# Performance work log

Measured on AMD Instinct MI355X. Metric: run time of the kernel, lower is better.

## Reference

```python
import jax, jax.numpy as jnp
import numpy as np

B, N, E = 32, 256, 300   # batch, num hyperedges, word emb size
H, K = 256, 8            # nhidden, nhead
MARGIN = 0.2


def setup_inputs() -> dict:
    key = jax.random.key(0)
    ks = jax.random.split(key, 10)
    s_in = 1.0 / np.sqrt(E)
    s_h = 1.0 / np.sqrt(H)
    s_fc = 1.0 / np.sqrt(H * K)
    return {
        'he_anchor': jax.random.normal(ks[0], (B, N, E), jnp.float32),
        'he_pos': jax.random.normal(ks[1], (B, N, E), jnp.float32),
        'he_neg': jax.random.normal(ks[2], (B, N, E), jnp.float32),
        'W_a2h': jax.random.uniform(ks[3], (H, E), jnp.float32, -s_in, s_in),
        'b_a2h': jax.random.uniform(ks[4], (H,), jnp.float32, -s_in, s_in),
        'W_c2h': jax.random.uniform(ks[5], (H, E), jnp.float32, -s_in, s_in),
        'b_c2h': jax.random.uniform(ks[6], (H,), jnp.float32, -s_in, s_in),
        'W_att': jax.random.uniform(ks[7], (K, H), jnp.float32, -s_h, s_h),
        'b_att': jax.random.uniform(ks[8], (K,), jnp.float32, -s_h, s_h),
        'W_fc': jax.random.uniform(ks[9], (1, H * K), jnp.float32, -s_fc, s_fc),
        'b_fc': jnp.zeros((1,), jnp.float32),
    }


def _score(x, y, W_a2h, b_a2h, W_c2h, b_c2h, W_att, b_att, W_fc, b_fc):
    # a2h / c2h projections, then permute to [B, H, N]
    Aa = jnp.transpose(x @ W_a2h.T + b_a2h, (0, 2, 1))  # [B,H,N]
    Ac = jnp.transpose(y @ W_c2h.T + b_c2h, (0, 2, 1))  # [B,H,M]
    # h2att applied to the outer product Aa[b,h,n]*Ac[b,h,m]; fuse into one einsum
    logits = jnp.einsum('bhn,bhm,kh->bknm', Aa, Ac, W_att) + b_att[None, :, None, None]
    b_, k_, n_, m_ = logits.shape
    att = jax.nn.softmax(logits.reshape(b_, k_, n_ * m_), axis=-1).reshape(b_, k_, n_, m_)
    # per-head bilinear aggregation: out[b,k,h] = sum_{n,m} Aa[b,h,n]*att[b,k,n,m]*Ac[b,h,m]
    t = jnp.einsum('bhn,bknm->bkhm', Aa, att)
    out = jnp.einsum('bkhm,bhm->bkh', t, Ac)
    # torch concat order is head-major: [B, K*H]
    out = out.reshape(b_, k_ * H)
    return out @ W_fc.T + b_fc  # [B,1]


def reference(he_anchor, he_pos, he_neg, W_a2h, b_a2h, W_c2h, b_c2h, W_att, b_att, W_fc, b_fc):
    score_p = _score(he_anchor, he_pos, W_a2h, b_a2h, W_c2h, b_c2h, W_att, b_att, W_fc, b_fc)
    score_n = _score(he_anchor, he_neg, W_a2h, b_a2h, W_c2h, b_c2h, W_att, b_att, W_fc, b_fc)
    loss = jnp.mean(jax.nn.relu(score_n - score_p + MARGIN))
    return loss
```

## Files before the change

kernel.cpp:

```cpp
#include <hip/hip_runtime.h>

#define BB 32
#define NN 256
#define EE 300
#define HH 256
#define KK 8
#define MARGINF 0.2f
#define EP 320

typedef __attribute__((ext_vector_type(8))) short bf16x8;
typedef __attribute__((ext_vector_type(4))) float f32x4;
typedef __attribute__((ext_vector_type(16))) float f32x16;

__device__ inline ushort f2bf(float f) {
  unsigned u = __float_as_uint(f);
  u += 0x7fffu + ((u >> 16) & 1u);
  return (ushort)(u >> 16);
}
__device__ inline float bf2f(ushort s) { return __uint_as_float(((unsigned)s) << 16); }
__device__ inline unsigned cvtpk(float lo, float hi) {
  unsigned r;
  asm("v_cvt_pk_bf16_f32 %0, %1, %2" : "=v"(r) : "v"(lo), "v"(hi));
  return r;
}
__device__ inline void gload_lds16(const ushort* g, ushort* l) {
  __builtin_amdgcn_global_load_lds(
      (const __attribute__((address_space(1))) void*)g,
      (__attribute__((address_space(3))) void*)l, 16, 0, 0);
}

__global__ __launch_bounds__(256) void wconv_kernel(
    const float* __restrict__ Wa, const float* __restrict__ Wc,
    ushort* __restrict__ Wt, unsigned* __restrict__ counter)
{
  const int i = blockIdx.x * 256 + threadIdx.x;
  if (i == 0) counter[0] = 0u;
  const int w = i / 81920;
  int r = i - w * 81920;
  const int hb = r / 5120; r -= hb * 5120;
  const int ks = r / 512;  r -= ks * 512;
  const int l = r >> 3, j = r & 7;
  const int h = hb * 16 + (l & 15);
  const int e = ks * 32 + (l >> 4) * 8 + j;
  const float* src = w ? Wc : Wa;
  Wt[i] = (e < EE) ? f2bf(src[h * EE + e]) : (ushort)0;
}

__global__ __launch_bounds__(256, 3) void proj_kernel(
    const float* __restrict__ he_a, const float* __restrict__ he_p,
    const float* __restrict__ he_n, const ushort* __restrict__ Wt,
    const float* __restrict__ b_a2h, const float* __restrict__ b_c2h,
    ushort* __restrict__ AT)
{
  const int z = blockIdx.y;
  const int which = z >> 5;
  const int b = z & 31;
  const int nb = blockIdx.x;
  const int n0 = nb * 32;
  const int tid = threadIdx.x;
  const int wv = tid >> 6;
  const int lane = tid & 63;
  const int col = lane & 15;
  const int quad = lane >> 4;

  const float* X = (which == 0 ? he_a : which == 1 ? he_p : he_n) + (size_t)b * NN * EE;
  const ushort* W = Wt + (size_t)(which == 0 ? 0 : 1) * 81920;
  const float* bias = (which == 0 ? b_a2h : b_c2h);

  __shared__ __align__(16) ushort sX[32][328];
  __shared__ __align__(16) ushort tr[32][264];

  {
    const int row = tid >> 3, seg = tid & 7;
    const float* xr = X + (size_t)(n0 + row) * EE;
#pragma unroll
    for (int q = 0; q < 10; q++) {
      const int jj = seg + 8 * q;
      float4 xv = {0.f, 0.f, 0.f, 0.f};
      if (jj < 75) xv = *(const float4*)&xr[4 * jj];
      uint2 p; p.x = cvtpk(xv.x, xv.y); p.y = cvtpk(xv.z, xv.w);
      *(uint2*)&sX[row][4 * jj] = p;
    }
  }
  __syncthreads();

  f32x4 acc[2][4];
#pragma unroll
  for (int nf = 0; nf < 2; nf++)
#pragma unroll
    for (int mb = 0; mb < 4; mb++) acc[nf][mb] = (f32x4){0.f, 0.f, 0.f, 0.f};

#pragma unroll
  for (int ks = 0; ks < 10; ks++) {
    const int off = 32 * ks + 8 * quad;
    const bf16x8 a0 = *(const bf16x8*)&sX[col][off];
    const bf16x8 a1 = *(const bf16x8*)&sX[16 + col][off];
#pragma unroll
    for (int mb = 0; mb < 4; mb++) {
      const bf16x8 w8 = *(const bf16x8*)&W[(4 * wv + mb) * 5120 + ks * 512 + lane * 8];
      acc[0][mb] = __builtin_amdgcn_mfma_f32_16x16x32_bf16(a0, w8, acc[0][mb], 0, 0, 0);
      acc[1][mb] = __builtin_amdgcn_mfma_f32_16x16x32_bf16(a1, w8, acc[1][mb], 0, 0, 0);
    }
  }

#pragma unroll
  for (int nf = 0; nf < 2; nf++)
#pragma unroll
    for (int mb = 0; mb < 4; mb++) {
      const float bi = bias[64 * wv + 16 * mb + col];
#pragma unroll
      for (int r = 0; r < 4; r++)
        tr[16 * nf + 4 * quad + r][64 * wv + 16 * mb + col] = f2bf(acc[nf][mb][r] + bi);
    }
  __syncthreads();
  {
    ushort* dst = AT + (size_t)(which * BB + b) * (NN * HH) + (size_t)nb * 8192;
#pragma unroll
    for (int it = 0; it < 4; it++) {
      const int c = it * 256 + tid;
      const int row = c & 31, hs = (c >> 5) & 1, hb = c >> 6;
      *(uint4*)&dst[c * 8] = *(const uint4*)&tr[row][hb * 16 + hs * 8];
    }
  }
}

__global__ __launch_bounds__(512, 1) void attn_kernel(
    const ushort* __restrict__ AT, const float* __restrict__ Watt,
    const float* __restrict__ Wfc, const float* __restrict__ bfc,
    float* __restrict__ scoresK, unsigned* __restrict__ counter,
    float* __restrict__ out)
{
  const int d = blockIdx.x;
  const int x = d & 7;
  const int j = d >> 3;
  const int grp = x * 8 + (j & 7);
  const int kp = j >> 3;
  const int which = grp >> 5;
  const int b = grp & 31;
  const int tid = threadIdx.x;
  const int wid = tid >> 6;
  const int kh = wid >> 2;
  const int ws = wid & 3;
  const int lane = tid & 63;
  const int k = 2 * kp + kh;

  const ushort* Ta = AT + (size_t)b * (NN * HH);
  const ushort* Tc = AT + (size_t)((1 + which) * BB + b) * (NN * HH);

  __shared__ __align__(16) ushort sB[65536];
  __shared__ __align__(16) ushort wkb[2][256];
  __shared__ __align__(16) ushort wfb[2][256];
  __shared__ float red[16];
  __shared__ unsigned isLast;

#pragma unroll
  for (int it = 0; it < 16; it++) {
    const int off = (wid * 16 + it) * 512;
    gload_lds16(Tc + off + lane * 8, &sB[off]);
  }
  {
    const int h = tid & 255, hd = tid >> 8;
    const int kt = 2 * kp + hd;
    wkb[hd][h] = f2bf(Watt[(size_t)kt * HH + h]);
    wfb[hd][h] = f2bf(Wfc[(size_t)kt * HH + h]);
  }
  __syncthreads();

  const ushort* wkp = wkb[kh];
  const ushort* wfp = wfb[kh];

  float num = 0.f, den = 0.f;

#pragma unroll 1
  for (int si = 0; si < 2; si++) {
    const int s = si ^ kh;
    bf16x8 saf[16], gaf[16];
    {
      const ushort* abase = Ta + (4 * s + ws) * 8192 + lane * 8;
#pragma unroll
      for (int ks = 0; ks < 16; ks++) {
        const bf16x8 a = *(const bf16x8*)&abase[ks * 512];
        const int off = 16 * ks + 8 * (lane >> 5);
        const bf16x8 w8 = *(const bf16x8*)&wkp[off];
        const bf16x8 f8 = *(const bf16x8*)&wfp[off];
        union { bf16x8 v; unsigned u[4]; } sv, gv;
#pragma unroll
        for (int jj = 0; jj < 4; jj++) {
          const float a0 = bf2f((ushort)a[2 * jj]), a1 = bf2f((ushort)a[2 * jj + 1]);
          sv.u[jj] = cvtpk(a0 * bf2f((ushort)w8[2 * jj]), a1 * bf2f((ushort)w8[2 * jj + 1]));
          gv.u[jj] = cvtpk(a0 * bf2f((ushort)f8[2 * jj]), a1 * bf2f((ushort)f8[2 * jj + 1]));
        }
        saf[ks] = sv.v; gaf[ks] = gv.v;
      }
    }

#pragma unroll 1
    for (int mi = 0; mi < 4; mi++) {
      const int mtp = (mi + ws) & 3;
      const int mbase = mtp * 16384;
      f32x16 aS0 = {0,0,0,0,0,0,0,0,0,0,0,0,0,0,0,0};
      f32x16 aG0 = {0,0,0,0,0,0,0,0,0,0,0,0,0,0,0,0};
      f32x16 aS1 = {0,0,0,0,0,0,0,0,0,0,0,0,0,0,0,0};
      f32x16 aG1 = {0,0,0,0,0,0,0,0,0,0,0,0,0,0,0,0};
      __builtin_amdgcn_s_setprio(1);
#pragma unroll
      for (int ks = 0; ks < 16; ks++) {
        const bf16x8 b0 = *(const bf16x8*)&sB[mbase + ks * 512 + lane * 8];
        const bf16x8 b1 = *(const bf16x8*)&sB[mbase + 8192 + ks * 512 + lane * 8];
        aS0 = __builtin_amdgcn_mfma_f32_32x32x16_bf16(saf[ks], b0, aS0, 0, 0, 0);
        aG0 = __builtin_amdgcn_mfma_f32_32x32x16_bf16(gaf[ks], b0, aG0, 0, 0, 0);
        aS1 = __builtin_amdgcn_mfma_f32_32x32x16_bf16(saf[ks], b1, aS1, 0, 0, 0);
        aG1 = __builtin_amdgcn_mfma_f32_32x32x16_bf16(gaf[ks], b1, aG1, 0, 0, 0);
      }
      __builtin_amdgcn_s_setprio(0);
#pragma unroll
      for (int r = 0; r < 16; r++) {
        const float p0 = __expf(aS0[r]);
        den += p0; num = fmaf(p0, aG0[r], num);
        const float p1 = __expf(aS1[r]);
        den += p1; num = fmaf(p1, aG1[r], num);
      }
    }
  }

#pragma unroll
  for (int off = 32; off >= 1; off >>= 1) {
    num += __shfl_xor(num, off);
    den += __shfl_xor(den, off);
  }
  if (lane == 0) { red[wid] = num; red[8 + wid] = den; }
  __syncthreads();
  if (tid == 0) {
    const float n0 = red[0] + red[1] + red[2] + red[3];
    const float d0 = red[8] + red[9] + red[10] + red[11];
    const float n1 = red[4] + red[5] + red[6] + red[7];
    const float d1 = red[12] + red[13] + red[14] + red[15];
    atomicExch(&scoresK[(2 * kp) * 64 + grp], n0 / d0);
    atomicExch(&scoresK[(2 * kp + 1) * 64 + grp], n1 / d1);
    __threadfence();
    isLast = (atomicAdd(counter, 1u) == 255u) ? 1u : 0u;
  }
  __syncthreads();

  if (isLast && tid < 64) {
    float s = bfc[0];
#pragma unroll
    for (int kk = 0; kk < KK; kk++)
      s += atomicAdd(&scoresK[kk * 64 + tid], 0.0f);
    const float other = __shfl(s, tid + 32);
    float v = 0.f;
    if (tid < 32) v = fmaxf(other - s + MARGINF, 0.f);
#pragma unroll
    for (int off = 32; off >= 1; off >>= 1) v += __shfl_xor(v, off);
    if (tid == 0) out[0] = v * (1.0f / 32.0f);
  }
}

extern "C" void kernel_launch(void* const* d_in, const int* in_sizes, int n_in,
                              void* d_out, int out_size, void* d_ws, size_t ws_size,
                              hipStream_t stream) {
  const float* he_a  = (const float*)d_in[0];
  const float* he_p  = (const float*)d_in[1];
  const float* he_n  = (const float*)d_in[2];
  const float* W_a2h = (const float*)d_in[3];
  const float* b_a2h = (const float*)d_in[4];
  const float* W_c2h = (const float*)d_in[5];
  const float* b_c2h = (const float*)d_in[6];
  const float* W_att = (const float*)d_in[7];
  const float* W_fc  = (const float*)d_in[9];
  const float* b_fc  = (const float*)d_in[10];

  ushort* AT = (ushort*)d_ws;
  float* scoresK = (float*)(AT + (size_t)3 * BB * NN * HH);
  ushort* Wt = (ushort*)(scoresK + 512);
  unsigned* counter = (unsigned*)(Wt + (size_t)2 * HH * EP);
  (void)ws_size; (void)in_sizes; (void)n_in; (void)out_size;

  wconv_kernel<<<640, 256, 0, stream>>>(W_a2h, W_c2h, Wt, counter);
  dim3 pg(8, 96);
  proj_kernel<<<pg, 256, 0, stream>>>(he_a, he_p, he_n, Wt, b_a2h, b_c2h, AT);
  attn_kernel<<<256, 512, 0, stream>>>(AT, W_att, W_fc, b_fc, scoresK, counter, (float*)d_out);
}
```

Baseline: 132.5 us.

## Software-pipeline MFMA clusters with exp tails and vectorize weight conversion

The attention kernel's inner loop now computes 32-column MFMA clusters one at a time and overlaps each cluster's MFMAs with the exp/softmax accumulation of the previous cluster, using two ping-pong accumulator pairs. The LDS start offset is rotated per wave across eight clusters. The aim is to hide the VALU exp work behind matrix-core work instead of running them back to back. The weight conversion kernel also handles four elements per thread with float4 loads and launches 4x fewer blocks. The setprio hints were removed, and the ping-pong scheme can raise register pressure.

After: 520.7 us. 3.93x slower.

```diff
diff --git a/kernel.cpp b/kernel.cpp
--- a/kernel.cpp
+++ b/kernel.cpp
@@ -35,15 +35,21 @@
 {
   const int i = blockIdx.x * 256 + threadIdx.x;
   if (i == 0) counter[0] = 0u;
-  const int w = i / 81920;
-  int r = i - w * 81920;
+  const int base = i * 4;
+  const int w = base / 81920;
+  int r = base - w * 81920;
   const int hb = r / 5120; r -= hb * 5120;
   const int ks = r / 512;  r -= ks * 512;
   const int l = r >> 3, j = r & 7;
   const int h = hb * 16 + (l & 15);
-  const int e = ks * 32 + (l >> 4) * 8 + j;
+  const int e0 = ks * 32 + (l >> 4) * 8 + j;
   const float* src = w ? Wc : Wa;
-  Wt[i] = (e < EE) ? f2bf(src[h * EE + e]) : (ushort)0;
+  ushort4 o = {0, 0, 0, 0};
+  if (e0 < EE) {
+    const float4 v = *(const float4*)&src[h * EE + e0];
+    o.x = f2bf(v.x); o.y = f2bf(v.y); o.z = f2bf(v.z); o.w = f2bf(v.w);
+  }
+  *(ushort4*)&Wt[base] = o;
 }
 
 __global__ __launch_bounds__(256, 3) void proj_kernel(
@@ -121,6 +127,29 @@
       const int row = c & 31, hs = (c >> 5) & 1, hb = c >> 6;
       *(uint4*)&dst[c * 8] = *(const uint4*)&tr[row][hb * 16 + hs * 8];
     }
+  }
+}
+
+__device__ __forceinline__ void cluster32(
+    const ushort* sBp, const bf16x8* saf, const bf16x8* gaf,
+    int mbase, int lane, f32x16& aS, f32x16& aG)
+{
+  aS = (f32x16){0,0,0,0,0,0,0,0,0,0,0,0,0,0,0,0};
+  aG = (f32x16){0,0,0,0,0,0,0,0,0,0,0,0,0,0,0,0};
+#pragma unroll
+  for (int ks = 0; ks < 16; ks++) {
+    const bf16x8 bv = *(const bf16x8*)&sBp[mbase + ks * 512 + lane * 8];
+    aS = __builtin_amdgcn_mfma_f32_32x32x16_bf16(saf[ks], bv, aS, 0, 0, 0);
+    aG = __builtin_amdgcn_mfma_f32_32x32x16_bf16(gaf[ks], bv, aG, 0, 0, 0);
+  }
+}
+__device__ __forceinline__ void tail32(
+    const f32x16& aS, const f32x16& aG, float& num, float& den)
+{
+#pragma unroll
+  for (int r = 0; r < 16; r++) {
+    const float p = __expf(aS[r]);
+    den += p; num = fmaf(p, aG[r], num);
   }
 }
 
@@ -142,7 +171,6 @@
   const int kh = wid >> 2;
   const int ws = wid & 3;
   const int lane = tid & 63;
-  const int k = 2 * kp + kh;
 
   const ushort* Ta = AT + (size_t)b * (NN * HH);
   const ushort* Tc = AT + (size_t)((1 + which) * BB + b) * (NN * HH);
@@ -194,33 +222,16 @@
       }
     }
 
-#pragma unroll 1
-    for (int mi = 0; mi < 4; mi++) {
-      const int mtp = (mi + ws) & 3;
-      const int mbase = mtp * 16384;
-      f32x16 aS0 = {0,0,0,0,0,0,0,0,0,0,0,0,0,0,0,0};
-      f32x16 aG0 = {0,0,0,0,0,0,0,0,0,0,0,0,0,0,0,0};
-      f32x16 aS1 = {0,0,0,0,0,0,0,0,0,0,0,0,0,0,0,0};
-      f32x16 aG1 = {0,0,0,0,0,0,0,0,0,0,0,0,0,0,0,0};
-      __builtin_amdgcn_s_setprio(1);
-#pragma unroll
-      for (int ks = 0; ks < 16; ks++) {
-        const bf16x8 b0 = *(const bf16x8*)&sB[mbase + ks * 512 + lane * 8];
-        const bf16x8 b1 = *(const bf16x8*)&sB[mbase + 8192 + ks * 512 + lane * 8];
-        aS0 = __builtin_amdgcn_mfma_f32_32x32x16_bf16(saf[ks], b0, aS0, 0, 0, 0);
-        aG0 = __builtin_amdgcn_mfma_f32_32x32x16_bf16(gaf[ks], b0, aG0, 0, 0, 0);
-        aS1 = __builtin_amdgcn_mfma_f32_32x32x16_bf16(saf[ks], b1, aS1, 0, 0, 0);
-        aG1 = __builtin_amdgcn_mfma_f32_32x32x16_bf16(gaf[ks], b1, aG1, 0, 0, 0);
-      }
-      __builtin_amdgcn_s_setprio(0);
-#pragma unroll
-      for (int r = 0; r < 16; r++) {
-        const float p0 = __expf(aS0[r]);
-        den += p0; num = fmaf(p0, aG0[r], num);
-        const float p1 = __expf(aS1[r]);
-        den += p1; num = fmaf(p1, aG1[r], num);
-      }
-    }
+    const int rot = 2 * ws + 4 * kh;
+    f32x16 aSA, aGA, aSB, aGB;
+    cluster32(sB, saf, gaf, ((0 + rot) & 7) * 8192, lane, aSA, aGA);
+#pragma unroll
+    for (int c = 1; c < 8; c++) {
+      const int mbase = ((c + rot) & 7) * 8192;
+      if (c & 1) { cluster32(sB, saf, gaf, mbase, lane, aSB, aGB); tail32(aSA, aGA, num, den); }
+      else       { cluster32(sB, saf, gaf, mbase, lane, aSA, aGA); tail32(aSB, aGB, num, den); }
+    }
+    tail32(aSB, aGB, num, den);
   }
 
 #pragma unroll
@@ -276,7 +287,7 @@
   unsigned* counter = (unsigned*)(Wt + (size_t)2 * HH * EP);
   (void)ws_size; (void)in_sizes; (void)n_in; (void)out_size;
 
-  wconv_kernel<<<640, 256, 0, stream>>>(W_a2h, W_c2h, Wt, counter);
+  wconv_kernel<<<160, 256, 0, stream>>>(W_a2h, W_c2h, Wt, counter);
   dim3 pg(8, 96);
   proj_kernel<<<pg, 256, 0, stream>>>(he_a, he_p, he_n, Wt, b_a2h, b_c2h, AT);
   attn_kernel<<<256, 512, 0, stream>>>(AT, W_att, W_fc, b_fc, scoresK, counter, (float*)d_out);
```
